# Optimization experiments

Hardware: AMD Instinct MI355X
Metric: run time of the kernel (lower is better)

Reference implementation:

```python
import jax, jax.numpy as jnp
import numpy as np

HEADS = 16
LN_EPS = 1e-5

def _ln(v, w, b):
    # LayerNorm over last dim (head dim s)
    mu = jnp.mean(v, axis=-1, keepdims=True)
    var = jnp.mean(jnp.square(v - mu), axis=-1, keepdims=True)
    return (v - mu) * jax.lax.rsqrt(var + LN_EPS) * w + b

def setup_inputs() -> dict:
    key = jax.random.key(0)
    ks = jax.random.split(key, 5)
    b, t, e = 2, 2048, 1024
    x = jax.random.normal(ks[0], (b, t, e), dtype=jnp.float32)
    scale = 0.02
    Wk = jax.random.normal(ks[1], (e, e), dtype=jnp.float32) * scale
    Wq = jax.random.normal(ks[2], (e, e), dtype=jnp.float32) * scale
    Wv = jax.random.normal(ks[3], (e, e), dtype=jnp.float32) * scale
    Wu = jax.random.normal(ks[4], (e, e), dtype=jnp.float32) * scale
    s = e // HEADS
    return {
        "x": x, "Wk": Wk, "Wq": Wq, "Wv": Wv, "Wu": Wu,
        "kln_w": jnp.ones((s,), jnp.float32), "kln_b": jnp.zeros((s,), jnp.float32),
        "qln_w": jnp.ones((s,), jnp.float32), "qln_b": jnp.zeros((s,), jnp.float32),
    }

def reference(x, Wk, Wq, Wv, Wu, kln_w, kln_b, qln_w, qln_b):
    b, t, e = x.shape
    h = HEADS
    s = e // h
    # nn.Linear: y = x @ W^T
    k = (x @ Wk.T).reshape(b, t, h, s)
    q = (x @ Wq.T).reshape(b, t, h, s)
    v = (x @ Wv.T).reshape(b, t, h, s)
    k = _ln(k, kln_w, kln_b)
    q = _ln(q, qln_w, qln_b)
    scalefactor = 1.0 / np.sqrt(s).astype(np.float32)
    # [b, h, t_q, t_k]
    dot = jnp.einsum('bqhs,bkhs->bhqk', q, k) * scalefactor
    causal = jnp.triu(jnp.ones((t, t), dtype=bool), k=1)  # mask strictly-upper (diag kept)
    dot = jnp.where(causal, -jnp.inf, dot)
    attn = jax.nn.softmax(dot, axis=-1)
    out = jnp.einsum('bhqk,bkhs->bqhs', attn, v).reshape(b, t, e)
    return out @ Wu.T
```

## Files before the change

### kernel.cpp

```cpp
#include <hip/hip_runtime.h>
#include <math.h>

#define T_SEQ 2048
#define E_DIM 1024
#define NH    16
#define HS    64
#define NB    2
#define M_ROWS 4096

typedef __attribute__((ext_vector_type(8))) short bf16x8;
typedef __attribute__((ext_vector_type(4))) float f32x4;

#define AS1 __attribute__((address_space(1)))
#define AS3 __attribute__((address_space(3)))

__device__ __forceinline__ ushort f2bf(float f) {
    union { float f; unsigned u; } c; c.f = f;
    unsigned r = c.u + 0x7fffu + ((c.u >> 16) & 1u);
    return (ushort)(r >> 16);
}

__device__ __forceinline__ void load_lds16(const ushort* g, ushort* l) {
    __builtin_amdgcn_global_load_lds((const AS1 unsigned int*)g,
                                     (AS3 unsigned int*)l, 16, 0, 0);
}

__global__ __launch_bounds__(256) void cvt_all(
    const float* __restrict__ x,  const float* __restrict__ Wk,
    const float* __restrict__ Wq, const float* __restrict__ Wv,
    const float* __restrict__ Wu,
    ushort* __restrict__ xb,  ushort* __restrict__ Wkb,
    ushort* __restrict__ Wqb, ushort* __restrict__ Wvb,
    ushort* __restrict__ Wub)
{
    int i4 = blockIdx.x * 256 + threadIdx.x;
    int region = i4 >> 18;
    const float* src; ushort* dst; int off;
    if      (region < 4)  { src = x;  dst = xb;  off = i4; }
    else if (region == 4) { src = Wk; dst = Wkb; off = i4 - (4 << 18); }
    else if (region == 5) { src = Wq; dst = Wqb; off = i4 - (5 << 18); }
    else if (region == 6) { src = Wv; dst = Wvb; off = i4 - (6 << 18); }
    else                  { src = Wu; dst = Wub; off = i4 - (7 << 18); }
    float4 v = *(const float4*)(src + (size_t)off * 4);
    ushort4 o; o.x = f2bf(v.x); o.y = f2bf(v.y); o.z = f2bf(v.z); o.w = f2bf(v.w);
    *(ushort4*)(dst + (size_t)off * 4) = o;
}

__device__ __forceinline__ void gemm_core(
    const ushort* __restrict__ A, const ushort* __restrict__ W,
    ushort* As, ushort* Bs, f32x4 acc[4][4])
{
    const int tid  = threadIdx.x;
    const int lane = tid & 63, w = tid >> 6;
    const int quad = lane >> 4, l16 = lane & 15;
    const int wm = w & 1, wn = w >> 1;
    const int m0 = blockIdx.y * 128, n0 = blockIdx.x * 128;

    const int rl   = lane >> 2;
    const int gsw  = (lane & 3) ^ ((lane >> 3) & 3);
    const int fsw  = (l16 >> 1) & 3;

    const f32x4 zero = {0.f, 0.f, 0.f, 0.f};
#pragma unroll
    for (int mt = 0; mt < 4; ++mt)
#pragma unroll
        for (int nt = 0; nt < 4; ++nt) acc[mt][nt] = zero;

    for (int k0 = 0; k0 < E_DIM; k0 += 32) {
#pragma unroll
        for (int i = 0; i < 2; ++i) {
            int c = i * 4 + w;
            int row = c * 16 + rl;
            load_lds16(A + (size_t)(m0 + row) * E_DIM + k0 + gsw * 8, As + c * 512);
            load_lds16(W + (size_t)(n0 + row) * E_DIM + k0 + gsw * 8, Bs + c * 512);
        }
        __syncthreads();
        bf16x8 af[4], bfr[4];
#pragma unroll
        for (int mt = 0; mt < 4; ++mt)
            af[mt] = *(const bf16x8*)(As + (wm * 64 + mt * 16 + l16) * 32
                                      + ((quad ^ fsw) * 8));
#pragma unroll
        for (int nt = 0; nt < 4; ++nt)
            bfr[nt] = *(const bf16x8*)(Bs + (wn * 64 + nt * 16 + l16) * 32
                                       + ((quad ^ fsw) * 8));
#pragma unroll
        for (int mt = 0; mt < 4; ++mt)
#pragma unroll
            for (int nt = 0; nt < 4; ++nt)
                acc[mt][nt] = __builtin_amdgcn_mfma_f32_16x16x32_bf16(
                    af[mt], bfr[nt], acc[mt][nt], 0, 0, 0);
        __syncthreads();
    }
}

__global__ __launch_bounds__(256) void gemm_qkv(
    const ushort* __restrict__ A,
    const ushort* __restrict__ W0, const ushort* __restrict__ W1,
    const ushort* __restrict__ W2,
    ushort* __restrict__ Kb, ushort* __restrict__ Qb, ushort* __restrict__ Vt,
    const float* __restrict__ kw, const float* __restrict__ kbias,
    const float* __restrict__ qw, const float* __restrict__ qbias)
{
    __shared__ ushort As[128 * 32];
    __shared__ ushort Bs[128 * 32];
    const int z = blockIdx.z;
    const ushort* W = (z == 0) ? W0 : (z == 1) ? W1 : W2;
    f32x4 acc[4][4];
    gemm_core(A, W, As, Bs, acc);

    const int lane = threadIdx.x & 63, w = threadIdx.x >> 6;
    const int quad = lane >> 4, l16 = lane & 15;
    const int wm = w & 1, wn = w >> 1;
    const int m0 = blockIdx.y * 128, n0 = blockIdx.x * 128;
    const int row0 = m0 + wm * 64;
    const int col0 = n0 + wn * 64;

    if (z < 2) {
        ushort* C = z ? Qb : Kb;
        const float* lw = z ? qw : kw;
        const float* lb = z ? qbias : kbias;
        const float scale = z ? 0.125f : 1.0f;
        float wv[4], bv_[4];
#pragma unroll
        for (int nt = 0; nt < 4; ++nt) {
            wv[nt]  = lw[nt * 16 + l16];
            bv_[nt] = lb[nt * 16 + l16];
        }
#pragma unroll
        for (int mt = 0; mt < 4; ++mt)
#pragma unroll
            for (int r = 0; r < 4; ++r) {
                float v[4], d[4];
#pragma unroll
                for (int nt = 0; nt < 4; ++nt) v[nt] = acc[mt][nt][r];
                float s = v[0] + v[1] + v[2] + v[3];
                s += __shfl_xor(s, 1); s += __shfl_xor(s, 2);
                s += __shfl_xor(s, 4); s += __shfl_xor(s, 8);
                float mu = s * (1.0f / 64.0f);
                float q2 = 0.f;
#pragma unroll
                for (int nt = 0; nt < 4; ++nt) { d[nt] = v[nt] - mu; q2 += d[nt] * d[nt]; }
                q2 += __shfl_xor(q2, 1); q2 += __shfl_xor(q2, 2);
                q2 += __shfl_xor(q2, 4); q2 += __shfl_xor(q2, 8);
                float rin = rsqrtf(q2 * (1.0f / 64.0f) + 1e-5f);
                int row = row0 + mt * 16 + quad * 4 + r;
#pragma unroll
                for (int nt = 0; nt < 4; ++nt)
                    C[(size_t)row * E_DIM + col0 + nt * 16 + l16] =
                        f2bf((d[nt] * rin * wv[nt] + bv_[nt]) * scale);
            }
    } else {
        const int bidx = m0 >> 11;
        const int hh   = col0 >> 6;
        const int t0   = (m0 & 2047) + wm * 64;
#pragma unroll
        for (int mt = 0; mt < 4; ++mt)
#pragma unroll
            for (int nt = 0; nt < 4; ++nt) {
                ushort4 pk = make_ushort4(f2bf(acc[mt][nt][0]), f2bf(acc[mt][nt][1]),
                                          f2bf(acc[mt][nt][2]), f2bf(acc[mt][nt][3]));
                size_t off = ((size_t)(bidx * NH + hh) * 64 + nt * 16 + l16) * T_SEQ
                             + t0 + mt * 16 + quad * 4;
                *(ushort4*)(Vt + off) = pk;
            }
    }
}

__global__ __launch_bounds__(256) void gemm_o(
    const ushort* __restrict__ A, const ushort* __restrict__ W,
    float* __restrict__ C)
{
    __shared__ ushort As[128 * 32];
    __shared__ ushort Bs[128 * 32];
    f32x4 acc[4][4];
    gemm_core(A, W, As, Bs, acc);

    const int lane = threadIdx.x & 63, w = threadIdx.x >> 6;
    const int quad = lane >> 4, l16 = lane & 15;
    const int row0 = blockIdx.y * 128 + (w & 1) * 64;
    const int col0 = blockIdx.x * 128 + (w >> 1) * 64;
#pragma unroll
    for (int mt = 0; mt < 4; ++mt)
#pragma unroll
        for (int nt = 0; nt < 4; ++nt)
#pragma unroll
            for (int r = 0; r < 4; ++r)
                C[(size_t)(row0 + mt * 16 + quad * 4 + r) * E_DIM
                  + col0 + nt * 16 + l16] = acc[mt][nt][r];
}

__global__ __launch_bounds__(256) void flash_attn2(
    const ushort* __restrict__ Qg, const ushort* __restrict__ Kg,
    const ushort* __restrict__ Vt, ushort* __restrict__ O)
{
    __shared__ ushort Ks[2][64 * 64];
    __shared__ ushort Vs[2][64 * 64];
    __shared__ ushort Ps[4][16 * 64];

    const int tid  = threadIdx.x;
    const int lane = tid & 63, w = tid >> 6;
    const int quad = lane >> 4, l16 = lane & 15;
    const int qt = blockIdx.x, bh = blockIdx.y;
    const int b = bh >> 4, h = bh & 15;

    const ushort* Qbase = Qg + ((size_t)b * T_SEQ) * E_DIM + h * HS;
    const ushort* Kbase = Kg + ((size_t)b * T_SEQ) * E_DIM + h * HS;
    const ushort* Vbase = Vt + ((size_t)bh * HS) * T_SEQ;

    const int rloc = lane >> 3;
    const int gswc = (lane & 7) ^ rloc;
    const int sw   = l16 & 7;

    bf16x8 aq[2];
#pragma unroll
    for (int ks = 0; ks < 2; ++ks)
        aq[ks] = *(const bf16x8*)(Qbase + (size_t)(qt * 64 + w * 16 + l16) * E_DIM
                                  + ks * 32 + quad * 8);

    const f32x4 zero = {0.f, 0.f, 0.f, 0.f};
    f32x4 o_acc[4];
#pragma unroll
    for (int dt = 0; dt < 4; ++dt) o_acc[dt] = zero;
    float l_acc[4] = {0.f, 0.f, 0.f, 0.f};

#pragma unroll
    for (int i = 0; i < 2; ++i) {
        int c = w * 2 + i, row = c * 8 + rloc;
        load_lds16(Kbase + (size_t)row * E_DIM + gswc * 8, Ks[0] + c * 512);
        load_lds16(Vbase + (size_t)row * T_SEQ + gswc * 8, Vs[0] + c * 512);
    }

    for (int jt = 0; jt <= qt; ++jt) {
        const int buf = jt & 1;
        __syncthreads();
        if (jt < qt) {
#pragma unroll
            for (int i = 0; i < 2; ++i) {
                int c = w * 2 + i, row = c * 8 + rloc;
                load_lds16(Kbase + (size_t)(jt + 1) * 64 * E_DIM
                           + (size_t)row * E_DIM + gswc * 8, Ks[buf ^ 1] + c * 512);
                load_lds16(Vbase + (size_t)row * T_SEQ + (jt + 1) * 64 + gswc * 8,
                           Vs[buf ^ 1] + c * 512);
            }
        }

        f32x4 sa[4];
#pragma unroll
        for (int nt = 0; nt < 4; ++nt) sa[nt] = zero;
#pragma unroll
        for (int ks = 0; ks < 2; ++ks) {
            int cp = ((ks * 4 + quad) ^ sw) * 8;
#pragma unroll
            for (int nt = 0; nt < 4; ++nt) {
                bf16x8 bk = *(const bf16x8*)(Ks[buf] + (nt * 16 + l16) * 64 + cp);
                sa[nt] = __builtin_amdgcn_mfma_f32_16x16x32_bf16(aq[ks], bk, sa[nt], 0, 0, 0);
            }
        }

        if (jt == qt) {
#pragma unroll
            for (int nt = 0; nt < 4; ++nt)
#pragma unroll
                for (int r = 0; r < 4; ++r)
                    if (nt * 16 + l16 > w * 16 + quad * 4 + r) sa[nt][r] = -1e30f;
        }

#pragma unroll
        for (int nt = 0; nt < 4; ++nt)
#pragma unroll
            for (int r = 0; r < 4; ++r) {
                float p = __expf(sa[nt][r] - 8.0f);
                sa[nt][r] = p;
                l_acc[r] += p;
            }

#pragma unroll
        for (int nt = 0; nt < 4; ++nt)
#pragma unroll
            for (int r = 0; r < 4; ++r) {
                int row = quad * 4 + r;
                int cp  = (nt * 2 + (l16 >> 3)) ^ (row & 7);
                Ps[w][row * 64 + cp * 8 + (l16 & 7)] = f2bf(sa[nt][r]);
            }

#pragma unroll
        for (int ks = 0; ks < 2; ++ks) {
            int cp = ((ks * 4 + quad) ^ sw) * 8;
            bf16x8 ap = *(const bf16x8*)(Ps[w] + l16 * 64 + cp);
#pragma unroll
            for (int dt = 0; dt < 4; ++dt) {
                bf16x8 bv = *(const bf16x8*)(Vs[buf] + (dt * 16 + l16) * 64 + cp);
                o_acc[dt] = __builtin_amdgcn_mfma_f32_16x16x32_bf16(ap, bv, o_acc[dt], 0, 0, 0);
            }
        }
    }

#pragma unroll
    for (int r = 0; r < 4; ++r) {
        float L = l_acc[r];
        L += __shfl_xor(L, 1); L += __shfl_xor(L, 2);
        L += __shfl_xor(L, 4); L += __shfl_xor(L, 8);
        float inv = 1.0f / L;
        int trow = qt * 64 + w * 16 + quad * 4 + r;
#pragma unroll
        for (int dt = 0; dt < 4; ++dt)
            O[((size_t)b * T_SEQ + trow) * E_DIM + h * HS + dt * 16 + l16] =
                f2bf(o_acc[dt][r] * inv);
    }
}

extern "C" void kernel_launch(void* const* d_in, const int* in_sizes, int n_in,
                              void* d_out, int out_size, void* d_ws, size_t ws_size,
                              hipStream_t stream) {
    const float* x     = (const float*)d_in[0];
    const float* Wk    = (const float*)d_in[1];
    const float* Wq    = (const float*)d_in[2];
    const float* Wv    = (const float*)d_in[3];
    const float* Wu    = (const float*)d_in[4];
    const float* kln_w = (const float*)d_in[5];
    const float* kln_b = (const float*)d_in[6];
    const float* qln_w = (const float*)d_in[7];
    const float* qln_b = (const float*)d_in[8];
    float* out = (float*)d_out;

    const size_t NE = (size_t)M_ROWS * E_DIM;
    const size_t NW = (size_t)E_DIM * E_DIM;
    ushort* xb  = (ushort*)d_ws;
    ushort* Wkb = xb  + NE;
    ushort* Wqb = Wkb + NW;
    ushort* Wvb = Wqb + NW;
    ushort* Wub = Wvb + NW;
    ushort* Kb  = Wub + NW;
    ushort* Qb  = Kb  + NE;
    ushort* Vt  = Qb  + NE;
    ushort* Ob  = Vt  + NE;

    cvt_all<<<8192, 256, 0, stream>>>(x, Wk, Wq, Wv, Wu, xb, Wkb, Wqb, Wvb, Wub);

    gemm_qkv<<<dim3(E_DIM / 128, M_ROWS / 128, 3), 256, 0, stream>>>(
        xb, Wkb, Wqb, Wvb, Kb, Qb, Vt, kln_w, kln_b, qln_w, qln_b);

    flash_attn2<<<dim3(T_SEQ / 64, NB * NH), 256, 0, stream>>>(Qb, Kb, Vt, Ob);

    gemm_o<<<dim3(E_DIM / 128, M_ROWS / 128), 256, 0, stream>>>(Ob, Wub, out);
}
```

Baseline: 224.8 us.

## Rebalance causal attention scheduling, use exp2 softmax, and shrink output GEMM tiles

Attention now launches as a 1D grid that interleaves short and long causal query tiles, so the triangular work is spread more evenly across CUs. The log2(e) factor is folded into the Q scale so the softmax uses the hardware exp2 instruction, and P is truncated to bf16 instead of rounded. The output projection GEMM switches to 128x64 tiles, doubling the block count to 512 so the GPU is filled better. The trade-off is slightly lower precision in P and less data reuse per block in gemm_o.

```diff
diff --git a/kernel.cpp b/kernel.cpp
--- a/kernel.cpp
+++ b/kernel.cpp
@@ -14,10 +14,16 @@
 #define AS1 __attribute__((address_space(1)))
 #define AS3 __attribute__((address_space(3)))
 
+#define LOG2E 1.4426950408889634f
+
 __device__ __forceinline__ ushort f2bf(float f) {
     union { float f; unsigned u; } c; c.f = f;
     unsigned r = c.u + 0x7fffu + ((c.u >> 16) & 1u);
     return (ushort)(r >> 16);
+}
+__device__ __forceinline__ ushort f2bf_trunc(float f) {
+    union { float f; unsigned u; } c; c.f = f;
+    return (ushort)(c.u >> 16);
 }
 
 __device__ __forceinline__ void load_lds16(const ushort* g, ushort* l) {
@@ -120,7 +126,7 @@
         ushort* C = z ? Qb : Kb;
         const float* lw = z ? qw : kw;
         const float* lb = z ? qbias : kbias;
-        const float scale = z ? 0.125f : 1.0f;
+        const float scale = z ? (0.125f * LOG2E) : 1.0f;
         float wv[4], bv_[4];
 #pragma unroll
         for (int nt = 0; nt < 4; ++nt) {
@@ -172,25 +178,67 @@
     float* __restrict__ C)
 {
     __shared__ ushort As[128 * 32];
-    __shared__ ushort Bs[128 * 32];
-    f32x4 acc[4][4];
-    gemm_core(A, W, As, Bs, acc);
-
-    const int lane = threadIdx.x & 63, w = threadIdx.x >> 6;
+    __shared__ ushort Bs[64 * 32];
+    const int tid  = threadIdx.x;
+    const int lane = tid & 63, w = tid >> 6;
     const int quad = lane >> 4, l16 = lane & 15;
-    const int row0 = blockIdx.y * 128 + (w & 1) * 64;
-    const int col0 = blockIdx.x * 128 + (w >> 1) * 64;
+    const int wm = w & 1, wn = w >> 1;
+    const int m0 = blockIdx.y * 128, n0 = blockIdx.x * 64;
+
+    const int rl  = lane >> 2;
+    const int gsw = (lane & 3) ^ ((lane >> 3) & 3);
+    const int fsw = (l16 >> 1) & 3;
+
+    const f32x4 zero = {0.f, 0.f, 0.f, 0.f};
+    f32x4 acc[4][2];
 #pragma unroll
     for (int mt = 0; mt < 4; ++mt)
 #pragma unroll
-        for (int nt = 0; nt < 4; ++nt)
+        for (int nt = 0; nt < 2; ++nt) acc[mt][nt] = zero;
+
+    for (int k0 = 0; k0 < E_DIM; k0 += 32) {
+#pragma unroll
+        for (int i = 0; i < 2; ++i) {
+            int c = i * 4 + w;
+            int row = c * 16 + rl;
+            load_lds16(A + (size_t)(m0 + row) * E_DIM + k0 + gsw * 8, As + c * 512);
+        }
+        {
+            int row = w * 16 + rl;
+            load_lds16(W + (size_t)(n0 + row) * E_DIM + k0 + gsw * 8, Bs + w * 512);
+        }
+        __syncthreads();
+        bf16x8 af[4], bfr[2];
+#pragma unroll
+        for (int mt = 0; mt < 4; ++mt)
+            af[mt] = *(const bf16x8*)(As + (wm * 64 + mt * 16 + l16) * 32
+                                      + ((quad ^ fsw) * 8));
+#pragma unroll
+        for (int nt = 0; nt < 2; ++nt)
+            bfr[nt] = *(const bf16x8*)(Bs + (wn * 32 + nt * 16 + l16) * 32
+                                       + ((quad ^ fsw) * 8));
+#pragma unroll
+        for (int mt = 0; mt < 4; ++mt)
+#pragma unroll
+            for (int nt = 0; nt < 2; ++nt)
+                acc[mt][nt] = __builtin_amdgcn_mfma_f32_16x16x32_bf16(
+                    af[mt], bfr[nt], acc[mt][nt], 0, 0, 0);
+        __syncthreads();
+    }
+
+    const int row0 = m0 + wm * 64;
+    const int col0 = n0 + wn * 32;
+#pragma unroll
+    for (int mt = 0; mt < 4; ++mt)
+#pragma unroll
+        for (int nt = 0; nt < 2; ++nt)
 #pragma unroll
             for (int r = 0; r < 4; ++r)
                 C[(size_t)(row0 + mt * 16 + quad * 4 + r) * E_DIM
                   + col0 + nt * 16 + l16] = acc[mt][nt][r];
 }
 
-__global__ __launch_bounds__(256) void flash_attn2(
+__global__ __launch_bounds__(256) void flash_attn3(
     const ushort* __restrict__ Qg, const ushort* __restrict__ Kg,
     const ushort* __restrict__ Vt, ushort* __restrict__ O)
 {
@@ -201,7 +249,13 @@
     const int tid  = threadIdx.x;
     const int lane = tid & 63, w = tid >> 6;
     const int quad = lane >> 4, l16 = lane & 15;
-    const int qt = blockIdx.x, bh = blockIdx.y;
+
+    const int L = blockIdx.x;
+    const int c = L & 255, s = L >> 8;
+    const int q0 = c >> 5;
+    const int bh = c & 31;
+    const int qt = (s == 0) ? q0 : (s == 1) ? (15 - q0)
+                 : (s == 2) ? (16 + q0) : (31 - q0);
     const int b = bh >> 4, h = bh & 15;
 
     const ushort* Qbase = Qg + ((size_t)b * T_SEQ) * E_DIM + h * HS;
@@ -226,10 +280,12 @@
 
 #pragma unroll
     for (int i = 0; i < 2; ++i) {
-        int c = w * 2 + i, row = c * 8 + rloc;
-        load_lds16(Kbase + (size_t)row * E_DIM + gswc * 8, Ks[0] + c * 512);
-        load_lds16(Vbase + (size_t)row * T_SEQ + gswc * 8, Vs[0] + c * 512);
-    }
+        int cc = w * 2 + i, row = cc * 8 + rloc;
+        load_lds16(Kbase + (size_t)row * E_DIM + gswc * 8, Ks[0] + cc * 512);
+        load_lds16(Vbase + (size_t)row * T_SEQ + gswc * 8, Vs[0] + cc * 512);
+    }
+
+    const float M8 = 8.0f * LOG2E;
 
     for (int jt = 0; jt <= qt; ++jt) {
         const int buf = jt & 1;
@@ -237,11 +293,11 @@
         if (jt < qt) {
 #pragma unroll
             for (int i = 0; i < 2; ++i) {
-                int c = w * 2 + i, row = c * 8 + rloc;
+                int cc = w * 2 + i, row = cc * 8 + rloc;
                 load_lds16(Kbase + (size_t)(jt + 1) * 64 * E_DIM
-                           + (size_t)row * E_DIM + gswc * 8, Ks[buf ^ 1] + c * 512);
+                           + (size_t)row * E_DIM + gswc * 8, Ks[buf ^ 1] + cc * 512);
                 load_lds16(Vbase + (size_t)row * T_SEQ + (jt + 1) * 64 + gswc * 8,
-                           Vs[buf ^ 1] + c * 512);
+                           Vs[buf ^ 1] + cc * 512);
             }
         }
 
@@ -270,7 +326,7 @@
         for (int nt = 0; nt < 4; ++nt)
 #pragma unroll
             for (int r = 0; r < 4; ++r) {
-                float p = __expf(sa[nt][r] - 8.0f);
+                float p = __builtin_amdgcn_exp2f(sa[nt][r] - M8);
                 sa[nt][r] = p;
                 l_acc[r] += p;
             }
@@ -281,7 +337,7 @@
             for (int r = 0; r < 4; ++r) {
                 int row = quad * 4 + r;
                 int cp  = (nt * 2 + (l16 >> 3)) ^ (row & 7);
-                Ps[w][row * 64 + cp * 8 + (l16 & 7)] = f2bf(sa[nt][r]);
+                Ps[w][row * 64 + cp * 8 + (l16 & 7)] = f2bf_trunc(sa[nt][r]);
             }
 
 #pragma unroll
@@ -298,10 +354,10 @@
 
 #pragma unroll
     for (int r = 0; r < 4; ++r) {
-        float L = l_acc[r];
-        L += __shfl_xor(L, 1); L += __shfl_xor(L, 2);
-        L += __shfl_xor(L, 4); L += __shfl_xor(L, 8);
-        float inv = 1.0f / L;
+        float Lr = l_acc[r];
+        Lr += __shfl_xor(Lr, 1); Lr += __shfl_xor(Lr, 2);
+        Lr += __shfl_xor(Lr, 4); Lr += __shfl_xor(Lr, 8);
+        float inv = 1.0f / Lr;
         int trow = qt * 64 + w * 16 + quad * 4 + r;
 #pragma unroll
         for (int dt = 0; dt < 4; ++dt)
@@ -341,7 +397,7 @@
     gemm_qkv<<<dim3(E_DIM / 128, M_ROWS / 128, 3), 256, 0, stream>>>(
         xb, Wkb, Wqb, Wvb, Kb, Qb, Vt, kln_w, kln_b, qln_w, qln_b);
 
-    flash_attn2<<<dim3(T_SEQ / 64, NB * NH), 256, 0, stream>>>(Qb, Kb, Vt, Ob);
-
-    gemm_o<<<dim3(E_DIM / 128, M_ROWS / 128), 256, 0, stream>>>(Ob, Wub, out);
-}
+    flash_attn3<<<1024, 256, 0, stream>>>(Qb, Kb, Vt, Ob);
+
+    gemm_o<<<dim3(E_DIM / 64, M_ROWS / 128), 256, 0, stream>>>(Ob, Wub, out);
+}
```

After: 189.3 us. 1.19x faster.
